# Kernel tuning notes

Hardware: AMD Instinct MI355X
Metric: run time of the kernel (lower is better)

Reference implementation:

```python
import jax, jax.numpy as jnp
import numpy as np

VOCAB = 32000; D_MODEL = 768; N_LAYERS = 4
D_STATE = 16; D_CONV = 4; EXPAND = 2
D_INNER = EXPAND * D_MODEL                 # 1536
DT_RANK = (D_MODEL + 15) // 16             # 48
BATCH = 2; SEQ = 1024


def setup_inputs():
    key = jax.random.key(0)
    ks = jax.random.split(key, 10)
    def nrm(k, shape, scale=0.02):
        return (jax.random.normal(k, shape) * scale).astype(jnp.float32)
    inp = {}
    inp['tokens'] = jax.random.randint(ks[0], (BATCH, SEQ), 0, VOCAB)
    inp['embedding'] = nrm(ks[1], (VOCAB, D_MODEL))
    inp['head_bias'] = jnp.zeros((VOCAB,), jnp.float32)
    inp['ln_g'] = jnp.ones((N_LAYERS, D_MODEL), jnp.float32)
    inp['ln_b'] = jnp.zeros((N_LAYERS, D_MODEL), jnp.float32)
    inp['W_in'] = nrm(ks[2], (N_LAYERS, 2 * D_INNER, D_MODEL))
    inp['conv_w'] = nrm(ks[3], (N_LAYERS, D_INNER, 1, D_CONV), 0.1)
    inp['conv_b'] = jnp.zeros((N_LAYERS, D_INNER), jnp.float32)
    inp['W_xproj'] = nrm(ks[4], (N_LAYERS, DT_RANK + 2 * D_STATE, D_INNER))
    inp['W_dt'] = nrm(ks[5], (N_LAYERS, D_INNER, DT_RANK), 0.1)
    inp['b_dt'] = nrm(ks[6], (N_LAYERS, D_INNER), 0.5)
    # S4D-real init: A_n = n for n in 1..d_state
    inp['A_log'] = jnp.broadcast_to(jnp.log(jnp.arange(1, D_STATE + 1, dtype=jnp.float32)), (N_LAYERS, D_INNER, D_STATE)).copy()
    inp['D_ssm'] = jnp.ones((N_LAYERS, D_INNER), jnp.float32)
    inp['W_out'] = nrm(ks[7], (N_LAYERS, D_MODEL, D_INNER))
    inp['norm_g'] = jnp.ones((D_MODEL,), jnp.float32)
    inp['norm_b'] = jnp.zeros((D_MODEL,), jnp.float32)
    return inp


def _ln(x, g, b):
    m = jnp.mean(x, axis=-1, keepdims=True)
    v = jnp.var(x, axis=-1, keepdims=True)
    return (x - m) * jax.lax.rsqrt(v + 1e-5) * g + b


def _mamba(x, W_in, conv_w, conv_b, W_xproj, W_dt, b_dt, A_log, D_ssm, W_out):
    # x: (S, B, D_MODEL)
    xz = jnp.einsum('sbd,ed->sbe', x, W_in)           # (S, B, 2*D_INNER)
    xc, z = jnp.split(xz, 2, axis=-1)
    # depthwise causal conv along sequence
    xt = jnp.transpose(xc, (1, 2, 0))                  # (B, C, S)
    xt = jax.lax.conv_general_dilated(xt, conv_w, (1,), [(D_CONV - 1, 0)],
                                      dimension_numbers=('NCH', 'OIH', 'NCH'),
                                      feature_group_count=D_INNER)
    xt = xt + conv_b[None, :, None]
    xc = jax.nn.silu(jnp.transpose(xt, (2, 0, 1)))     # (S, B, C)
    xdb = jnp.einsum('sbc,ec->sbe', xc, W_xproj)       # (S, B, DT_RANK+2N)
    dt_r = xdb[..., :DT_RANK]
    Bm = xdb[..., DT_RANK:DT_RANK + D_STATE]
    Cm = xdb[..., DT_RANK + D_STATE:]
    dt = jax.nn.softplus(jnp.einsum('sbr,cr->sbc', dt_r, W_dt) + b_dt)
    A = -jnp.exp(A_log)                                # (C, N)

    def step(h, t):
        dt_t, B_t, C_t, x_t = t                        # (B,C),(B,N),(B,N),(B,C)
        dA = jnp.exp(dt_t[..., None] * A)              # (B, C, N)
        h = h * dA + (dt_t * x_t)[..., None] * B_t[:, None, :]
        y = jnp.einsum('bcn,bn->bc', h, C_t)
        return h, y

    h0 = jnp.zeros((x.shape[1], D_INNER, D_STATE), x.dtype)
    _, ys = jax.lax.scan(step, h0, (dt, Bm, Cm, xc))   # ys: (S, B, C)
    y = (ys + D_ssm * xc) * jax.nn.silu(z)
    return jnp.einsum('sbc,dc->sbd', y, W_out)


def reference(tokens, embedding, head_bias, ln_g, ln_b, W_in, conv_w, conv_b, W_xproj, W_dt, b_dt, A_log, D_ssm, W_out, norm_g, norm_b):
    x = embedding[tokens.T]                            # (S, B, D)
    for i in range(N_LAYERS):
        x = x + _mamba(_ln(x, ln_g[i], ln_b[i]), W_in[i], conv_w[i], conv_b[i],
                       W_xproj[i], W_dt[i], b_dt[i], A_log[i], D_ssm[i], W_out[i])
    x = _ln(x, norm_g, norm_b)
    logits = jnp.einsum('sbd,vd->sbv', x, embedding) + head_bias  # tied head
    return jnp.transpose(logits, (1, 0, 2))            # (B, S, VOCAB)
```

## Files before the change

### kernel.cpp

```cpp
#include <hip/hip_runtime.h>
#include <hip/hip_bf16.h>
#include <cstdint>
#include <cstddef>

#define SEQ_LEN 1024
#define NBATCH  2
#define MROWS   2048
#define DMODEL  768
#define DINNER  1536
#define DTRANK  48
#define DSTATE  16
#define NLAYERS 4
#define NVOCAB  32000
#define XPROJ_N 80
#define NCHUNK  16
#define CHUNK   64
#define GROUPS  (NBATCH * DINNER)
#define SCANW   (GROUPS * DSTATE)
#define XSPLIT  8

typedef __attribute__((ext_vector_type(4))) float f32x4;
typedef __attribute__((ext_vector_type(8))) short s16x8;
using bf16 = __hip_bfloat16;

__device__ __forceinline__ float b2f(bf16 v){ return __bfloat162float(v); }
__device__ __forceinline__ bf16  f2b(float v){ return __float2bfloat16(v); }
__device__ __forceinline__ short f2bs(float v){
  return (short)__builtin_bit_cast(unsigned short, __float2bfloat16(v));
}

__device__ __forceinline__ void glds16(const ushort* g, ushort* l) {
  __builtin_amdgcn_global_load_lds(
      (const __attribute__((address_space(1))) void*)g,
      (__attribute__((address_space(3))) void*)l,
      16, 0, 0);
}

__global__ __launch_bounds__(256) void k_cvt(const float* __restrict__ in,
    ushort* __restrict__ out, int n4) {
  int i = blockIdx.x * 256 + threadIdx.x;
  if (i >= n4) return;
  f32x4 v = *(const f32x4*)(in + (size_t)i * 4);
  ushort4 o;
  o.x = (ushort)f2bs(v[0]); o.y = (ushort)f2bs(v[1]);
  o.z = (ushort)f2bs(v[2]); o.w = (ushort)f2bs(v[3]);
  *(ushort4*)(out + (size_t)i * 4) = o;
}

__global__ __launch_bounds__(256) void k_xsum(const float* __restrict__ p,
    ushort* __restrict__ out, int n4) {
  int i = blockIdx.x * 256 + threadIdx.x;
  if (i >= n4) return;
  f32x4 s = {};
#pragma unroll
  for (int z = 0; z < XSPLIT; z++) {
    f32x4 v = *(const f32x4*)(p + (size_t)z * (MROWS * XPROJ_N) + (size_t)i * 4);
    s[0] += v[0]; s[1] += v[1]; s[2] += v[2]; s[3] += v[3];
  }
  ushort4 o;
  o.x = (ushort)f2bs(s[0]); o.y = (ushort)f2bs(s[1]);
  o.z = (ushort)f2bs(s[2]); o.w = (ushort)f2bs(s[3]);
  *(ushort4*)(out + (size_t)i * 4) = o;
}

__global__ __launch_bounds__(256) void k_embed(const int* __restrict__ tok,
    const float* __restrict__ emb, float* __restrict__ x) {
  int id = blockIdx.x * 256 + threadIdx.x;
  int m = id / DMODEL, d = id - m * DMODEL;
  x[id] = emb[(size_t)tok[m] * DMODEL + d];
}

__global__ __launch_bounds__(256) void k_ln(const float* __restrict__ x,
    bf16* __restrict__ out, const float* __restrict__ g, const float* __restrict__ b) {
  int m = blockIdx.x;
  const float* row = x + (size_t)m * DMODEL;
  int t = threadIdx.x;
  float v0[3];
  float s = 0.f, s2 = 0.f;
#pragma unroll
  for (int j = 0; j < 3; j++) {
    float v = row[t + j * 256];
    v0[j] = v; s += v; s2 += v * v;
  }
#pragma unroll
  for (int o = 32; o >= 1; o >>= 1) { s += __shfl_xor(s, o); s2 += __shfl_xor(s2, o); }
  __shared__ float red[8];
  int wave = t >> 6;
  if ((t & 63) == 0) { red[wave] = s; red[4 + wave] = s2; }
  __syncthreads();
  s  = red[0] + red[1] + red[2] + red[3];
  s2 = red[4] + red[5] + red[6] + red[7];
  float mean = s * (1.f / DMODEL);
  float var  = s2 * (1.f / DMODEL) - mean * mean;
  float rstd = rsqrtf(var + 1e-5f);
#pragma unroll
  for (int j = 0; j < 3; j++) {
    int d = t + j * 256;
    float o = (v0[j] - mean) * rstd * g[d] + b[d];
    out[(size_t)m * DMODEL + d] = f2b(o);
  }
}

template<bool HAS_BIAS, bool ADD_TO_C, bool ATOMIC>
__global__ __launch_bounds__(256) void k_gemm128(
    const ushort* __restrict__ A, int lda,
    const ushort* __restrict__ B, int ldb,
    float* __restrict__ C, int ldc,
    const float* __restrict__ bias,
    int M, int N, int K)
{
  __shared__ ushort As[2][128 * 32];
  __shared__ ushort Bs[2][128 * 32];
  const int t = threadIdx.x;
  const int lane = t & 63;
  const int wave = t >> 6;
  const int tile_m = blockIdx.x * 128;
  const int tile_n = blockIdx.y * 128;
  const int kper = K / gridDim.z;
  const int kb = blockIdx.z * kper;
  const int ke = kb + kper;
  const int wr = (wave >> 1) * 64;
  const int wc = (wave & 1) * 64;

  f32x4 acc[4][4] = {};

  const int sr = wave * 32 + (lane >> 2);
  const int sc = (lane & 3) * 8;
  const ushort* gA0 = A + (size_t)(tile_m + sr) * lda + sc + kb;
  const ushort* gA1 = gA0 + (size_t)16 * lda;
  const ushort* gB0 = B + (size_t)(tile_n + sr) * ldb + sc + kb;
  const ushort* gB1 = gB0 + (size_t)16 * ldb;

  const int fr = lane & 15;
  const int kk = (lane >> 4) * 8;

  auto stage = [&](int bb) {
    glds16(gA0, &As[bb][wave * 1024]);
    glds16(gA1, &As[bb][wave * 1024 + 512]);
    glds16(gB0, &Bs[bb][wave * 1024]);
    glds16(gB1, &Bs[bb][wave * 1024 + 512]);
    gA0 += 32; gA1 += 32; gB0 += 32; gB1 += 32;
  };

  stage(0);
  int cur = 0;

  for (int k0 = kb; k0 < ke; k0 += 32) {
    if (k0 + 32 < ke) {
      stage(cur ^ 1);
      asm volatile("s_waitcnt vmcnt(4)" ::: "memory");
    } else {
      asm volatile("s_waitcnt vmcnt(0)" ::: "memory");
    }
    __builtin_amdgcn_s_barrier();

    s16x8 a[4], b[4];
#pragma unroll
    for (int m = 0; m < 4; m++)
      a[m] = *(const s16x8*)&As[cur][(wr + m * 16 + fr) * 32 + kk];
#pragma unroll
    for (int n = 0; n < 4; n++)
      b[n] = *(const s16x8*)&Bs[cur][(wc + n * 16 + fr) * 32 + kk];
#pragma unroll
    for (int m = 0; m < 4; m++)
#pragma unroll
      for (int n = 0; n < 4; n++)
        acc[m][n] = __builtin_amdgcn_mfma_f32_16x16x32_bf16(a[m], b[n], acc[m][n], 0, 0, 0);

    __builtin_amdgcn_s_barrier();
    cur ^= 1;
  }

  const int rq = (lane >> 4) * 4;
#pragma unroll
  for (int m = 0; m < 4; m++)
#pragma unroll
    for (int n = 0; n < 4; n++) {
      int colg = tile_n + wc + n * 16 + fr;
      float bv = HAS_BIAS ? bias[colg] : 0.f;
#pragma unroll
      for (int r = 0; r < 4; r++) {
        int rowg = tile_m + wr + m * 16 + rq + r;
        size_t idx = (size_t)rowg * ldc + colg;
        float v = acc[m][n][r] + bv;
        if constexpr (ATOMIC) atomicAdd(&C[idx], v);
        else if constexpr (ADD_TO_C) C[idx] += v;
        else C[idx] = v;
      }
    }
}

template<int MODE>
__global__ __launch_bounds__(256) void k_gemm(
    const ushort* __restrict__ A, int lda,
    const ushort* __restrict__ W, int ldw,
    void* __restrict__ Cout, int ldc,
    int M, int N, int K,
    const float* __restrict__ bias,
    const float* __restrict__ xcp,
    float* __restrict__ dtxp)
{
  __shared__ ushort As[64][40];
  __shared__ ushort Ws[64][40];
  const int tile_m = blockIdx.x * 64;
  const int tile_n = blockIdx.y * 64;
  const int t = threadIdx.x;
  const int lane = t & 63;
  const int wave = t >> 6;
  const int wr = (wave >> 1) * 32;
  const int wc = (wave & 1) * 32;
  f32x4 acc[2][2] = {};

  const int kper = ((K + gridDim.z - 1) / gridDim.z + 31) & ~31;
  const int kb = blockIdx.z * kper;
  int ke = kb + kper; if (ke > K) ke = K;

  const int srow = t >> 2;
  const int scol = (t & 3) * 8;

  for (int k0 = kb; k0 < ke; k0 += 32) {
    {
      int gm = tile_m + srow, gk = k0 + scol;
      s16x8 v = {};
      if (gm < M) {
        if (gk + 8 <= K) v = *(const s16x8*)(A + (size_t)gm * lda + gk);
        else {
#pragma unroll
          for (int j = 0; j < 8; j++) if (gk + j < K) v[j] = (short)A[(size_t)gm * lda + gk + j];
        }
      }
      *(s16x8*)&As[srow][scol] = v;
    }
    {
      int gn = tile_n + srow, gk = k0 + scol;
      s16x8 v = {};
      if (gn < N) {
        if (gk + 8 <= K) v = *(const s16x8*)(W + (size_t)gn * ldw + gk);
        else {
#pragma unroll
          for (int j = 0; j < 8; j++) if (gk + j < K) v[j] = (short)W[(size_t)gn * ldw + gk + j];
        }
      }
      *(s16x8*)&Ws[srow][scol] = v;
    }
    __syncthreads();
    const int kk = (lane >> 4) * 8;
    const int fr = lane & 15;
    s16x8 a0 = *(const s16x8*)&As[wr + fr][kk];
    s16x8 a1 = *(const s16x8*)&As[wr + 16 + fr][kk];
    s16x8 b0 = *(const s16x8*)&Ws[wc + fr][kk];
    s16x8 b1 = *(const s16x8*)&Ws[wc + 16 + fr][kk];
    acc[0][0] = __builtin_amdgcn_mfma_f32_16x16x32_bf16(a0, b0, acc[0][0], 0, 0, 0);
    acc[0][1] = __builtin_amdgcn_mfma_f32_16x16x32_bf16(a0, b1, acc[0][1], 0, 0, 0);
    acc[1][0] = __builtin_amdgcn_mfma_f32_16x16x32_bf16(a1, b0, acc[1][0], 0, 0, 0);
    acc[1][1] = __builtin_amdgcn_mfma_f32_16x16x32_bf16(a1, b1, acc[1][1], 0, 0, 0);
    __syncthreads();
  }

  const int fr = lane & 15;
  const int rq = (lane >> 4) * 4;
#pragma unroll
  for (int i = 0; i < 2; i++)
#pragma unroll
    for (int j = 0; j < 2; j++) {
      int colg = tile_n + wc + j * 16 + fr;
#pragma unroll
      for (int r = 0; r < 4; r++) {
        int rowg = tile_m + wr + i * 16 + rq + r;
        if (rowg < M && colg < N) {
          float v = acc[i][j][r];
          size_t idx = (size_t)rowg * ldc + colg;
          if constexpr (MODE == 0) {
            ((bf16*)Cout)[idx] = f2b(v);
          } else if constexpr (MODE == 2) {
            v += bias[colg];
            float sp = (v > 20.f) ? v : log1pf(__expf(v));
            ((float*)Cout)[idx] = sp;
            dtxp[idx] = sp * xcp[idx];
          } else {
            ((float*)Cout)[(size_t)blockIdx.z * (MROWS * XPROJ_N) + idx] = v;
          }
        }
      }
    }
}

__global__ __launch_bounds__(256) void k_conv(const float* __restrict__ xz,
    const float* __restrict__ w, const float* __restrict__ cb,
    float* __restrict__ xc, bf16* __restrict__ xcb) {
  int id = blockIdx.x * 256 + threadIdx.x;
  int m = id / DINNER, c = id - m * DINNER;
  int s = m & (SEQ_LEN - 1);
  float acc = cb[c];
#pragma unroll
  for (int k = 0; k < 4; k++) {
    int sp = s - 3 + k;
    if (sp >= 0) acc += w[c * 4 + k] * xz[(size_t)(m - 3 + k) * (2 * DINNER) + c];
  }
  float sil = acc / (1.f + __expf(-acc));
  xc[id] = sil;
  xcb[id] = f2b(sil);
}

__global__ __launch_bounds__(256) void k_scan1(const float* __restrict__ dt,
    const float* __restrict__ dtx, const bf16* __restrict__ xdb,
    const float* __restrict__ A_log, float* __restrict__ aprod,
    float* __restrict__ hend) {
  int gid = blockIdx.x * 256 + threadIdx.x;
  int n  = gid & 15;
  int t2 = gid >> 4;
  int j  = t2 / GROUPS;
  int cb = t2 - j * GROUPS;
  int c  = cb % DINNER;
  int b  = cb / DINNER;
  float Acn = -__expf(A_log[c * DSTATE + n]);
  float h = 0.f, ap = 1.f;
  int mbase = b * SEQ_LEN + j * CHUNK;
#pragma unroll 4
  for (int s = 0; s < CHUNK; s++) {
    int m = mbase + s;
    float dtv = dt[(size_t)m * DINNER + c];
    float dxv = dtx[(size_t)m * DINNER + c];
    float Bv  = b2f(xdb[(size_t)m * XPROJ_N + DTRANK + n]);
    float dA  = __expf(dtv * Acn);
    h = h * dA + dxv * Bv;
    ap *= dA;
  }
  aprod[gid] = ap;
  hend[gid]  = h;
}

__global__ __launch_bounds__(256) void k_scan2(const float* __restrict__ aprod,
    const float* __restrict__ hend, float* __restrict__ hin) {
  int idx = blockIdx.x * 256 + threadIdx.x;
  float h = 0.f;
#pragma unroll
  for (int j = 0; j < NCHUNK; j++) {
    hin[(size_t)j * SCANW + idx] = h;
    h = aprod[(size_t)j * SCANW + idx] * h + hend[(size_t)j * SCANW + idx];
  }
}

__global__ __launch_bounds__(256) void k_scan3(const float* __restrict__ dt,
    const float* __restrict__ dtx, const bf16* __restrict__ xdb,
    const float* __restrict__ A_log, const float* __restrict__ hin,
    float* __restrict__ y) {
  int gid = blockIdx.x * 256 + threadIdx.x;
  int n  = gid & 15;
  int t2 = gid >> 4;
  int j  = t2 / GROUPS;
  int cb = t2 - j * GROUPS;
  int c  = cb % DINNER;
  int b  = cb / DINNER;
  float Acn = -__expf(A_log[c * DSTATE + n]);
  float h = hin[gid];
  int mbase = b * SEQ_LEN + j * CHUNK;
#pragma unroll 2
  for (int s = 0; s < CHUNK; s++) {
    int m = mbase + s;
    float dtv = dt[(size_t)m * DINNER + c];
    float dxv = dtx[(size_t)m * DINNER + c];
    float Bv  = b2f(xdb[(size_t)m * XPROJ_N + DTRANK + n]);
    float Cv  = b2f(xdb[(size_t)m * XPROJ_N + DTRANK + DSTATE + n]);
    float dA  = __expf(dtv * Acn);
    h = h * dA + dxv * Bv;
    float p = h * Cv;
    p += __shfl_xor(p, 8);
    p += __shfl_xor(p, 4);
    p += __shfl_xor(p, 2);
    p += __shfl_xor(p, 1);
    if (n == 0) y[(size_t)m * DINNER + c] = p;
  }
}

__global__ __launch_bounds__(256) void k_ycomb(const float* __restrict__ y,
    const float* __restrict__ xc, const float* __restrict__ xz,
    const float* __restrict__ D_ssm, bf16* __restrict__ ybf) {
  int id = blockIdx.x * 256 + threadIdx.x;
  int m = id / DINNER, c = id - m * DINNER;
  float z = xz[(size_t)m * (2 * DINNER) + DINNER + c];
  float sil = z / (1.f + __expf(-z));
  float v = (y[id] + D_ssm[c] * xc[id]) * sil;
  ybf[id] = f2b(v);
}

extern "C" void kernel_launch(void* const* d_in, const int* in_sizes, int n_in,
                              void* d_out, int out_size, void* d_ws, size_t ws_size,
                              hipStream_t stream) {
  const int*   tokens    = (const int*)  d_in[0];
  const float* embedding = (const float*)d_in[1];
  const float* head_bias = (const float*)d_in[2];
  const float* ln_g      = (const float*)d_in[3];
  const float* ln_b      = (const float*)d_in[4];
  const float* W_in      = (const float*)d_in[5];
  const float* conv_w    = (const float*)d_in[6];
  const float* conv_b    = (const float*)d_in[7];
  const float* W_xproj   = (const float*)d_in[8];
  const float* W_dt      = (const float*)d_in[9];
  const float* b_dt      = (const float*)d_in[10];
  const float* A_log     = (const float*)d_in[11];
  const float* D_ssm     = (const float*)d_in[12];
  const float* W_out     = (const float*)d_in[13];
  const float* norm_g    = (const float*)d_in[14];
  const float* norm_b    = (const float*)d_in[15];
  float* out = (float*)d_out;

  char* ws = (char*)d_ws;
  size_t off = 0;
  auto alloc = [&](size_t bytes) -> char* {
    char* p = ws + off;
    off = (off + bytes + 255) & ~(size_t)255;
    return p;
  };
  float*  x     = (float*) alloc((size_t)MROWS * DMODEL * 4);
  bf16*   xln   = (bf16*)  alloc((size_t)MROWS * DMODEL * 2);
  float*  xz    = (float*) alloc((size_t)MROWS * 2 * DINNER * 4);
  float*  xc    = (float*) alloc((size_t)MROWS * DINNER * 4);
  bf16*   xcb   = (bf16*)  alloc((size_t)MROWS * DINNER * 2);
  bf16*   xdb   = (bf16*)  alloc((size_t)MROWS * XPROJ_N * 2);
  float*  xdbp  = (float*) alloc((size_t)XSPLIT * MROWS * XPROJ_N * 4);
  float*  dtf   = (float*) alloc((size_t)MROWS * DINNER * 4);
  float*  dtx   = (float*) alloc((size_t)MROWS * DINNER * 4);
  float*  yraw  = (float*) alloc((size_t)MROWS * DINNER * 4);
  bf16*   ybf   = (bf16*)  alloc((size_t)MROWS * DINNER * 2);
  float*  aprod = (float*) alloc((size_t)SCANW * NCHUNK * 4);
  float*  hend  = (float*) alloc((size_t)SCANW * NCHUNK * 4);
  float*  hin   = (float*) alloc((size_t)SCANW * NCHUNK * 4);
  ushort* ebf   = (ushort*)alloc((size_t)NVOCAB * DMODEL * 2);
  ushort* winb  = (ushort*)alloc((size_t)NLAYERS * 2 * DINNER * DMODEL * 2);
  ushort* wxpb  = (ushort*)alloc((size_t)NLAYERS * XPROJ_N * DINNER * 2);
  ushort* wdtb  = (ushort*)alloc((size_t)NLAYERS * DINNER * DTRANK * 2);
  ushort* woutb = (ushort*)alloc((size_t)NLAYERS * DMODEL * DINNER * 2);
  (void)ws_size; (void)in_sizes; (void)n_in; (void)out_size;

  auto cvt = [&](const float* src, ushort* dst, size_t n) {
    int n4 = (int)(n / 4);
    k_cvt<<<(n4 + 255) / 256, 256, 0, stream>>>(src, dst, n4);
  };
  cvt(embedding, ebf,   (size_t)NVOCAB * DMODEL);
  cvt(W_in,      winb,  (size_t)NLAYERS * 2 * DINNER * DMODEL);
  cvt(W_xproj,   wxpb,  (size_t)NLAYERS * XPROJ_N * DINNER);
  cvt(W_dt,      wdtb,  (size_t)NLAYERS * DINNER * DTRANK);
  cvt(W_out,     woutb, (size_t)NLAYERS * DMODEL * DINNER);

  k_embed<<<MROWS * DMODEL / 256, 256, 0, stream>>>(tokens, embedding, x);

  const int XDBN4 = MROWS * XPROJ_N / 4;

  for (int L = 0; L < NLAYERS; L++) {
    k_ln<<<MROWS, 256, 0, stream>>>(x, xln, ln_g + L * DMODEL, ln_b + L * DMODEL);

    k_gemm128<false, false, false><<<dim3(MROWS / 128, (2 * DINNER) / 128), 256, 0, stream>>>(
        (const ushort*)xln, DMODEL,
        winb + (size_t)L * 2 * DINNER * DMODEL, DMODEL,
        xz, 2 * DINNER, nullptr, MROWS, 2 * DINNER, DMODEL);

    k_conv<<<MROWS * DINNER / 256, 256, 0, stream>>>(
        xz, conv_w + (size_t)L * DINNER * 4, conv_b + (size_t)L * DINNER, xc, xcb);

    k_gemm<3><<<dim3(MROWS / 64, 2, XSPLIT), 256, 0, stream>>>(
        (const ushort*)xcb, DINNER,
        wxpb + (size_t)L * XPROJ_N * DINNER, DINNER,
        (void*)xdbp, XPROJ_N, MROWS, XPROJ_N, DINNER,
        nullptr, nullptr, nullptr);
    k_xsum<<<(XDBN4 + 255) / 256, 256, 0, stream>>>(xdbp, (ushort*)xdb, XDBN4);

    k_gemm<2><<<dim3(MROWS / 64, DINNER / 64), 256, 0, stream>>>(
        (const ushort*)xdb, XPROJ_N,
        wdtb + (size_t)L * DINNER * DTRANK, DTRANK,
        (void*)dtf, DINNER, MROWS, DINNER, DTRANK,
        b_dt + (size_t)L * DINNER, xc, dtx);

    const float* Al = A_log + (size_t)L * DINNER * DSTATE;
    k_scan1<<<SCANW * NCHUNK / 256, 256, 0, stream>>>(dtf, dtx, xdb, Al, aprod, hend);
    k_scan2<<<SCANW / 256, 256, 0, stream>>>(aprod, hend, hin);
    k_scan3<<<SCANW * NCHUNK / 256, 256, 0, stream>>>(dtf, dtx, xdb, Al, hin, yraw);

    k_ycomb<<<MROWS * DINNER / 256, 256, 0, stream>>>(
        yraw, xc, xz, D_ssm + (size_t)L * DINNER, ybf);

    k_gemm128<false, true, true><<<dim3(MROWS / 128, DMODEL / 128, 4), 256, 0, stream>>>(
        (const ushort*)ybf, DINNER,
        woutb + (size_t)L * DMODEL * DINNER, DINNER,
        x, DMODEL, nullptr, MROWS, DMODEL, DINNER);
  }

  k_ln<<<MROWS, 256, 0, stream>>>(x, xln, norm_g, norm_b);

  k_gemm128<true, false, false><<<dim3(MROWS / 128, NVOCAB / 128), 256, 0, stream>>>(
      (const ushort*)xln, DMODEL,
      ebf, DMODEL,
      out, NVOCAB, head_bias, MROWS, NVOCAB, DMODEL);
}
```

Measured before the change: 1.014 ms.

## Use 256x256 tile GEMM for LM head and fuse small prologue kernels

```diff
diff --git a/kernel.cpp b/kernel.cpp
--- a/kernel.cpp
+++ b/kernel.cpp
@@ -36,15 +36,33 @@
       16, 0, 0);
 }
 
-__global__ __launch_bounds__(256) void k_cvt(const float* __restrict__ in,
-    ushort* __restrict__ out, int n4) {
+#define CVT_E0 6144000
+#define CVT_E1 (CVT_E0 + 2359296)
+#define CVT_E2 (CVT_E1 + 1179648)
+#define CVT_E3 (CVT_E2 + 122880)
+#define CVT_E4 (CVT_E3 + 73728)
+__global__ __launch_bounds__(256) void k_cvt5(
+    const float* __restrict__ s0, const float* __restrict__ s1,
+    const float* __restrict__ s2, const float* __restrict__ s3,
+    const float* __restrict__ s4,
+    ushort* __restrict__ d0, ushort* __restrict__ d1,
+    ushort* __restrict__ d2, ushort* __restrict__ d3,
+    ushort* __restrict__ d4)
+{
   int i = blockIdx.x * 256 + threadIdx.x;
-  if (i >= n4) return;
-  f32x4 v = *(const f32x4*)(in + (size_t)i * 4);
+  const float* s; ushort* d; int base;
+  if      (i < CVT_E0) { s = s0; d = d0; base = 0; }
+  else if (i < CVT_E1) { s = s1; d = d1; base = CVT_E0; }
+  else if (i < CVT_E2) { s = s2; d = d2; base = CVT_E1; }
+  else if (i < CVT_E3) { s = s3; d = d3; base = CVT_E2; }
+  else if (i < CVT_E4) { s = s4; d = d4; base = CVT_E3; }
+  else return;
+  int li = i - base;
+  f32x4 v = *(const f32x4*)(s + (size_t)li * 4);
   ushort4 o;
   o.x = (ushort)f2bs(v[0]); o.y = (ushort)f2bs(v[1]);
   o.z = (ushort)f2bs(v[2]); o.w = (ushort)f2bs(v[3]);
-  *(ushort4*)(out + (size_t)i * 4) = o;
+  *(ushort4*)(d + (size_t)li * 4) = o;
 }
 
 __global__ __launch_bounds__(256) void k_xsum(const float* __restrict__ p,
@@ -63,25 +81,12 @@
   *(ushort4*)(out + (size_t)i * 4) = o;
 }
 
-__global__ __launch_bounds__(256) void k_embed(const int* __restrict__ tok,
-    const float* __restrict__ emb, float* __restrict__ x) {
-  int id = blockIdx.x * 256 + threadIdx.x;
-  int m = id / DMODEL, d = id - m * DMODEL;
-  x[id] = emb[(size_t)tok[m] * DMODEL + d];
-}
-
-__global__ __launch_bounds__(256) void k_ln(const float* __restrict__ x,
-    bf16* __restrict__ out, const float* __restrict__ g, const float* __restrict__ b) {
-  int m = blockIdx.x;
-  const float* row = x + (size_t)m * DMODEL;
-  int t = threadIdx.x;
-  float v0[3];
+__device__ __forceinline__ void ln_rows(const float v0[3], int t,
+    const float* __restrict__ g, const float* __restrict__ b,
+    bf16* __restrict__ outrow) {
   float s = 0.f, s2 = 0.f;
 #pragma unroll
-  for (int j = 0; j < 3; j++) {
-    float v = row[t + j * 256];
-    v0[j] = v; s += v; s2 += v * v;
-  }
+  for (int j = 0; j < 3; j++) { s += v0[j]; s2 += v0[j] * v0[j]; }
 #pragma unroll
   for (int o = 32; o >= 1; o >>= 1) { s += __shfl_xor(s, o); s2 += __shfl_xor(s2, o); }
   __shared__ float red[8];
@@ -96,9 +101,34 @@
 #pragma unroll
   for (int j = 0; j < 3; j++) {
     int d = t + j * 256;
-    float o = (v0[j] - mean) * rstd * g[d] + b[d];
-    out[(size_t)m * DMODEL + d] = f2b(o);
-  }
+    outrow[d] = f2b((v0[j] - mean) * rstd * g[d] + b[d]);
+  }
+}
+
+__global__ __launch_bounds__(256) void k_ln(const float* __restrict__ x,
+    bf16* __restrict__ out, const float* __restrict__ g, const float* __restrict__ b) {
+  int m = blockIdx.x;
+  const float* row = x + (size_t)m * DMODEL;
+  int t = threadIdx.x;
+  float v0[3];
+#pragma unroll
+  for (int j = 0; j < 3; j++) v0[j] = row[t + j * 256];
+  ln_rows(v0, t, g, b, out + (size_t)m * DMODEL);
+}
+
+__global__ __launch_bounds__(256) void k_embed_ln(const int* __restrict__ tok,
+    const float* __restrict__ emb, float* __restrict__ x,
+    bf16* __restrict__ out, const float* __restrict__ g, const float* __restrict__ b) {
+  int m = blockIdx.x;
+  const float* row = emb + (size_t)tok[m] * DMODEL;
+  int t = threadIdx.x;
+  float v0[3];
+#pragma unroll
+  for (int j = 0; j < 3; j++) {
+    v0[j] = row[t + j * 256];
+    x[(size_t)m * DMODEL + t + j * 256] = v0[j];
+  }
+  ln_rows(v0, t, g, b, out + (size_t)m * DMODEL);
 }
 
 template<bool HAS_BIAS, bool ADD_TO_C, bool ATOMIC>
@@ -186,6 +216,88 @@
         if constexpr (ATOMIC) atomicAdd(&C[idx], v);
         else if constexpr (ADD_TO_C) C[idx] += v;
         else C[idx] = v;
+      }
+    }
+}
+
+template<bool HAS_BIAS>
+__global__ __launch_bounds__(512) void k_gemm256(
+    const ushort* __restrict__ A, int lda,
+    const ushort* __restrict__ B, int ldb,
+    float* __restrict__ C, int ldc,
+    const float* __restrict__ bias,
+    int M, int N, int K)
+{
+  __shared__ ushort As[2][256 * 32];
+  __shared__ ushort Bs[2][256 * 32];
+  const int t = threadIdx.x;
+  const int lane = t & 63;
+  const int wave = t >> 6;
+  const int tile_m = blockIdx.x * 256;
+  const int tile_n = blockIdx.y * 256;
+  const int wr = (wave >> 2) * 128;
+  const int wc = (wave & 3) * 64;
+
+  f32x4 acc[8][4] = {};
+
+  const int sr = wave * 16 + (lane >> 2);
+  const int sc = (lane & 3) * 8;
+  const ushort* gA0 = A + (size_t)(tile_m + sr) * lda + sc;
+  const ushort* gA1 = A + (size_t)(tile_m + 128 + sr) * lda + sc;
+  const ushort* gB0 = B + (size_t)(tile_n + sr) * ldb + sc;
+  const ushort* gB1 = B + (size_t)(tile_n + 128 + sr) * ldb + sc;
+
+  const int fr = lane & 15;
+  const int kk = (lane >> 4) * 8;
+
+  auto stage = [&](int bb) {
+    glds16(gA0, &As[bb][wave * 512]);
+    glds16(gA1, &As[bb][4096 + wave * 512]);
+    glds16(gB0, &Bs[bb][wave * 512]);
+    glds16(gB1, &Bs[bb][4096 + wave * 512]);
+    gA0 += 32; gA1 += 32; gB0 += 32; gB1 += 32;
+  };
+
+  stage(0);
+  int cur = 0;
+
+  for (int k0 = 0; k0 < K; k0 += 32) {
+    if (k0 + 32 < K) {
+      stage(cur ^ 1);
+      asm volatile("s_waitcnt vmcnt(4)" ::: "memory");
+    } else {
+      asm volatile("s_waitcnt vmcnt(0)" ::: "memory");
+    }
+    __builtin_amdgcn_s_barrier();
+
+    s16x8 a[8], b[4];
+#pragma unroll
+    for (int m = 0; m < 8; m++)
+      a[m] = *(const s16x8*)&As[cur][(wr + m * 16 + fr) * 32 + kk];
+#pragma unroll
+    for (int n = 0; n < 4; n++)
+      b[n] = *(const s16x8*)&Bs[cur][(wc + n * 16 + fr) * 32 + kk];
+#pragma unroll
+    for (int m = 0; m < 8; m++)
+#pragma unroll
+      for (int n = 0; n < 4; n++)
+        acc[m][n] = __builtin_amdgcn_mfma_f32_16x16x32_bf16(a[m], b[n], acc[m][n], 0, 0, 0);
+
+    __builtin_amdgcn_s_barrier();
+    cur ^= 1;
+  }
+
+  const int rq = (lane >> 4) * 4;
+#pragma unroll
+  for (int m = 0; m < 8; m++)
+#pragma unroll
+    for (int n = 0; n < 4; n++) {
+      int colg = tile_n + wc + n * 16 + fr;
+      float bv = HAS_BIAS ? bias[colg] : 0.f;
+#pragma unroll
+      for (int r = 0; r < 4; r++) {
+        int rowg = tile_m + wr + m * 16 + rq + r;
+        C[(size_t)rowg * ldc + colg] = acc[m][n][r] + bv;
       }
     }
 }
@@ -433,22 +545,17 @@
   ushort* woutb = (ushort*)alloc((size_t)NLAYERS * DMODEL * DINNER * 2);
   (void)ws_size; (void)in_sizes; (void)n_in; (void)out_size;
 
-  auto cvt = [&](const float* src, ushort* dst, size_t n) {
-    int n4 = (int)(n / 4);
-    k_cvt<<<(n4 + 255) / 256, 256, 0, stream>>>(src, dst, n4);
-  };
-  cvt(embedding, ebf,   (size_t)NVOCAB * DMODEL);
-  cvt(W_in,      winb,  (size_t)NLAYERS * 2 * DINNER * DMODEL);
-  cvt(W_xproj,   wxpb,  (size_t)NLAYERS * XPROJ_N * DINNER);
-  cvt(W_dt,      wdtb,  (size_t)NLAYERS * DINNER * DTRANK);
-  cvt(W_out,     woutb, (size_t)NLAYERS * DMODEL * DINNER);
-
-  k_embed<<<MROWS * DMODEL / 256, 256, 0, stream>>>(tokens, embedding, x);
+  k_cvt5<<<(CVT_E4 + 255) / 256, 256, 0, stream>>>(
+      embedding, W_in, W_out, W_xproj, W_dt,
+      ebf, winb, woutb, wxpb, wdtb);
+
+  k_embed_ln<<<MROWS, 256, 0, stream>>>(tokens, embedding, x, xln, ln_g, ln_b);
 
   const int XDBN4 = MROWS * XPROJ_N / 4;
 
   for (int L = 0; L < NLAYERS; L++) {
-    k_ln<<<MROWS, 256, 0, stream>>>(x, xln, ln_g + L * DMODEL, ln_b + L * DMODEL);
+    if (L > 0)
+      k_ln<<<MROWS, 256, 0, stream>>>(x, xln, ln_g + L * DMODEL, ln_b + L * DMODEL);
 
     k_gemm128<false, false, false><<<dim3(MROWS / 128, (2 * DINNER) / 128), 256, 0, stream>>>(
         (const ushort*)xln, DMODEL,
@@ -487,7 +594,7 @@
 
   k_ln<<<MROWS, 256, 0, stream>>>(x, xln, norm_g, norm_b);
 
-  k_gemm128<true, false, false><<<dim3(MROWS / 128, NVOCAB / 128), 256, 0, stream>>>(
+  k_gemm256<true><<<dim3(MROWS / 256, NVOCAB / 256), 512, 0, stream>>>(
       (const ushort*)xln, DMODEL,
       ebf, DMODEL,
       out, NVOCAB, head_bias, MROWS, NVOCAB, DMODEL);
```

New measurement: 1.009 ms. No clear change (-0.5%).
